# Kernel tuning notes

Hardware: AMD Instinct MI355X
Metric: run time of the kernel (lower is better)

The kernel has to match this reference:

```python
import jax, jax.numpy as jnp
import numpy as np

B, C, P, H, W, S = 4, 256, 128, 56, 56, 5
EPS = 1e-5


def setup_inputs() -> dict:
    key = jax.random.key(0)
    ks = jax.random.split(key, 6)
    return {
        "x": jax.random.normal(ks[0], (B, C, H, W), jnp.float32),
        "Wt": jax.random.normal(ks[1], (P, C), jnp.float32) * 0.05,
        "Wp": jax.random.normal(ks[2], (P, C), jnp.float32) * 0.05,
        "Wg": jax.random.normal(ks[3], (S, P, C), jnp.float32) * 0.05,
        "W1": jax.random.normal(ks[4], (S, C, P), jnp.float32) * 0.05,
        "W2": jax.random.normal(ks[5], (S, C, P), jnp.float32) * 0.05,
        "gamma": jnp.ones((S, C), jnp.float32),
        "beta": jnp.zeros((S, C), jnp.float32),
    }


def _batchnorm(o, g, b):
    # training-mode BN over (batch, spatial); o: [b, C, n]
    mean = o.mean(axis=(0, 2), keepdims=True)
    var = ((o - mean) ** 2).mean(axis=(0, 2), keepdims=True)
    return (o - mean) * jax.lax.rsqrt(var + EPS) * g[None, :, None] + b[None, :, None]


def reference(x, Wt, Wp, Wg, W1, W2, gamma, beta):
    b, c, h, w = x.shape
    n = h * w
    xf = x.reshape(b, c, n)
    # 1x1 conv projections == channel matmuls
    t = jax.nn.relu(jnp.einsum('pc,bcn->bpn', Wt, xf))  # is_norm branch uses relu
    p = jax.nn.relu(jnp.einsum('pc,bcn->bpn', Wp, xf))
    att = jnp.einsum('bpi,bpj->bij', t, p)              # [b, n, n] affinity
    att = 0.5 * (att + jnp.swapaxes(att, 1, 2))         # is_sys symmetrization
    d = att.sum(axis=2)                                  # degree [b, n]
    d_safe = jnp.where(d != 0, d, 1.0)
    d_inv = jnp.where(d != 0, jax.lax.rsqrt(d_safe), 0.0)
    att = att * d_inv[:, None, :] * d_inv[:, :, None]    # D^-1/2 A D^-1/2
    out = xf
    for s in range(S):  # fixed small stage count
        g = jnp.einsum('pc,bcn->bpn', Wg[s], out)        # [b, P, n]
        ag = jnp.einsum('bij,bpj->bpi', att, g)          # att @ g over spatial
        o = jnp.einsum('cp,bpn->bcn', W1[s], ag) + jnp.einsum('cp,bpn->bcn', W2[s], g)
        out = _batchnorm(o, gamma[s], beta[s]) + out     # BN + residual
    return out.reshape(b, c, h, w)
```

## Files before the change

kernel.cpp:

```cpp
#include <hip/hip_runtime.h>

namespace {

constexpr int Bc = 4;
constexpr int Cc = 256;
constexpr int Pc = 128;
constexpr int NcT = 3136;
constexpr int Np = 3200;
constexpr int Sc = 5;
constexpr int KSn = 5;
constexpr int KCH = 640;
constexpr float EPSc = 1e-5f;

typedef __attribute__((ext_vector_type(8))) short bf16x8;
typedef __attribute__((ext_vector_type(4))) float f32x4;
typedef __attribute__((ext_vector_type(8))) unsigned short u16x8;
typedef __attribute__((ext_vector_type(4))) unsigned short u16x4;

__device__ inline float bf2f(unsigned short u) {
    return __uint_as_float(((unsigned)u) << 16);
}
__device__ inline unsigned short f2bf(float f) {
    unsigned u = __float_as_uint(f);
    return (unsigned short)((u + 0x7FFFu + ((u >> 16) & 1u)) >> 16);
}

template <int MT, int EPI, int CMOUT, bool SPLITK, int BNSTAT, bool F32OUT,
          bool FUSEBN>
__global__ __launch_bounds__(256) void mgemm(
    const unsigned short* __restrict__ A, int lda, long aB,
    const unsigned short* __restrict__ Bw, int ldb, long bB,
    unsigned short* __restrict__ outSM, int ldsm, long smB, long smSlice,
    unsigned short* __restrict__ outCM, long cmB,
    float* __restrict__ ps, float* __restrict__ ps2,
    int K, int kchunk, const float* __restrict__ dinv,
    const unsigned short* __restrict__ oin, const float* __restrict__ bnsc,
    const float* __restrict__ bnsh, float* __restrict__ resid)
{
    constexpr int TBA = MT * 64 * 2;
    constexpr int TBB = 128 * 64 * 2;
    constexpr int BUF = TBA + TBB;
    constexpr int OTB = MT * 132 * 4;
    constexpr int LDSZ = (2 * BUF > OTB + 2048) ? 2 * BUF : (OTB + 2048);
    __shared__ __align__(16) char lds[LDSZ];

    int b, kstart, kend;
    long smOff;
    if (SPLITK) {
        b = blockIdx.z & 3;
        int ks = blockIdx.z >> 2;
        kstart = ks * kchunk;
        kend = kstart + kchunk;
        smOff = (long)ks * smSlice;
    } else {
        b = blockIdx.z; kstart = 0; kend = K; smOff = 0;
    }
    const int n0 = blockIdx.x * 128;
    const int m0 = blockIdx.y * MT;
    const int tid = threadIdx.x;
    const int w = tid >> 6, l = tid & 63;

    const unsigned short* Ab = A + (size_t)b * aB + (size_t)m0 * lda;
    const unsigned short* Bb = Bw + (size_t)b * bB + (size_t)n0 * ldb;

    const int srow8 = tid >> 3;
    const int sgran = tid & 7;
    const int sswz = (sgran ^ (srow8 & 7)) * 8;
    constexpr int AR = MT / 32;

    constexpr int WC = (MT == 128) ? 2 : 4;
    constexpr int NB = 128 / WC / 16;
    const int wr = w / WC, wc = w % WC;

    f32x4 acc[4][NB] = {};
    float fup[AR][8];

    auto stageA = [&](int buf, int k0) {
        char* base = lds + buf * BUF;
#pragma unroll
        for (int j = 0; j < AR; ++j)
            __builtin_amdgcn_global_load_lds(
                (const __attribute__((address_space(1))) void*)
                    (Ab + (size_t)(j * 32 + srow8) * lda + k0 + sswz),
                (__attribute__((address_space(3))) void*)(base + j * 4096 + tid * 16),
                16, 0, 0);
    };
    auto stageB = [&](int buf, int k0) {
        char* base = lds + buf * BUF + TBA;
#pragma unroll
        for (int j = 0; j < 4; ++j)
            __builtin_amdgcn_global_load_lds(
                (const __attribute__((address_space(1))) void*)
                    (Bb + (size_t)(j * 32 + srow8) * ldb + k0 + sswz),
                (__attribute__((address_space(3))) void*)(base + j * 4096 + tid * 16),
                16, 0, 0);
    };
    auto fbLoad = [&](int k0) {
        const float* scp = bnsc + k0 + sgran * 8;
        const float* shp = bnsh + k0 + sgran * 8;
        float4 s0 = *(const float4*)scp, s1 = *(const float4*)(scp + 4);
        float4 h0 = *(const float4*)shp, h1 = *(const float4*)(shp + 4);
#pragma unroll
        for (int j = 0; j < AR; ++j) {
            int row = j * 32 + srow8;
            int n = m0 + row;
            size_t off = ((size_t)b * Np + n) * 256 + k0 + sgran * 8;
            if (n < NcT) {
                u16x8 ov = *(const u16x8*)(oin + off);
                float4 r0 = *(const float4*)(resid + off);
                float4 r1 = *(const float4*)(resid + off + 4);
                fup[j][0] = r0.x + fmaf(bf2f(ov[0]), s0.x, h0.x);
                fup[j][1] = r0.y + fmaf(bf2f(ov[1]), s0.y, h0.y);
                fup[j][2] = r0.z + fmaf(bf2f(ov[2]), s0.z, h0.z);
                fup[j][3] = r0.w + fmaf(bf2f(ov[3]), s0.w, h0.w);
                fup[j][4] = r1.x + fmaf(bf2f(ov[4]), s1.x, h1.x);
                fup[j][5] = r1.y + fmaf(bf2f(ov[5]), s1.y, h1.y);
                fup[j][6] = r1.z + fmaf(bf2f(ov[6]), s1.z, h1.z);
                fup[j][7] = r1.w + fmaf(bf2f(ov[7]), s1.w, h1.w);
            } else {
#pragma unroll
                for (int i = 0; i < 8; ++i) fup[j][i] = 0.f;
            }
            float4 w0, w1;
            w0.x = fup[j][0]; w0.y = fup[j][1]; w0.z = fup[j][2]; w0.w = fup[j][3];
            w1.x = fup[j][4]; w1.y = fup[j][5]; w1.z = fup[j][6]; w1.w = fup[j][7];
            *(float4*)(resid + off) = w0;
            *(float4*)(resid + off + 4) = w1;
        }
    };
    auto fbWrite = [&](int buf) {
        char* base = lds + buf * BUF;
#pragma unroll
        for (int j = 0; j < AR; ++j) {
            int row = j * 32 + srow8;
            u16x8 hv;
#pragma unroll
            for (int i = 0; i < 8; ++i) hv[i] = f2bf(fup[j][i]);
            *(u16x8*)(base + row * 128 + ((sgran ^ (row & 7)) << 4)) = hv;
        }
    };

    auto compute = [&](int buf) {
        const char* base = lds + buf * BUF;
        const int lo = l & 15, gq = l >> 4;
#pragma unroll
        for (int kh = 0; kh < 2; ++kh) {
            const int lg = kh * 4 + gq;
            bf16x8 bf[NB];
#pragma unroll
            for (int c = 0; c < NB; ++c) {
                int brow = wc * (16 * NB) + c * 16 + lo;
                bf[c] = *(const bf16x8*)(base + TBA + brow * 128 +
                                         ((lg ^ (brow & 7)) << 4));
            }
#pragma unroll
            for (int r = 0; r < 4; ++r) {
                int arow = wr * 64 + r * 16 + lo;
                bf16x8 af = *(const bf16x8*)(base + arow * 128 +
                                             ((lg ^ (arow & 7)) << 4));
#pragma unroll
                for (int c = 0; c < NB; ++c)
                    acc[r][c] = __builtin_amdgcn_mfma_f32_16x16x32_bf16(
                        af, bf[c], acc[r][c], 0, 0, 0);
            }
        }
    };

    const int nst = (kend - kstart) >> 6;
    if constexpr (FUSEBN) {
        fbLoad(kstart);
        fbWrite(0);
        stageB(0, kstart);
        __syncthreads();
        for (int s = 0; s < nst; ++s) {
            if (s + 1 < nst) {
                fbLoad(kstart + ((s + 1) << 6));
                stageB((s + 1) & 1, kstart + ((s + 1) << 6));
            }
            compute(s & 1);
            if (s + 1 < nst) fbWrite((s + 1) & 1);
            __syncthreads();
        }
    } else {
        stageA(0, kstart);
        stageB(0, kstart);
        __syncthreads();
        for (int s = 0; s < nst; ++s) {
            if (s + 1 < nst) {
                stageA((s + 1) & 1, kstart + ((s + 1) << 6));
                stageB((s + 1) & 1, kstart + ((s + 1) << 6));
            }
            compute(s & 1);
            __syncthreads();
        }
    }

    float* ot = (float*)lds;
    {
        const int lo = l & 15, gq = l >> 4;
#pragma unroll
        for (int r = 0; r < 4; ++r)
#pragma unroll
            for (int c = 0; c < NB; ++c)
#pragma unroll
                for (int j = 0; j < 4; ++j) {
                    float v = acc[r][c][j];
                    if (EPI == 1) v = fmaxf(v, 0.f);
                    ot[(wr * 64 + r * 16 + gq * 4 + j) * 132 +
                       wc * (16 * NB) + c * 16 + lo] = v;
                }
    }
    __syncthreads();

    {
        constexpr int TPR = 256 / MT;
        const int r = tid / TPR;
        const int c0 = (tid % TPR) * (MT / 2);
        if (F32OUT) {
            float* dst = (float*)outSM + (size_t)b * smB + smOff +
                         (size_t)(m0 + r) * ldsm + n0 + c0;
#pragma unroll
            for (int k = 0; k < MT / 8; ++k) {
                float4 v;
                v.x = ot[r * 132 + c0 + 4 * k + 0];
                v.y = ot[r * 132 + c0 + 4 * k + 1];
                v.z = ot[r * 132 + c0 + 4 * k + 2];
                v.w = ot[r * 132 + c0 + 4 * k + 3];
                *(float4*)(dst + 4 * k) = v;
            }
        } else {
            float sc = 1.f;
            if (EPI == 2) sc = 0.5f * dinv[(size_t)b * Np + m0 + r];
            unsigned short* dst = outSM + (size_t)b * smB + smOff +
                                  (size_t)(m0 + r) * ldsm + n0 + c0;
#pragma unroll
            for (int k = 0; k < MT / 16; ++k) {
                u16x8 o;
#pragma unroll
                for (int j = 0; j < 8; ++j) {
                    float v = ot[r * 132 + c0 + 8 * k + j];
                    if (EPI == 2) v *= sc;
                    o[j] = f2bf(v);
                }
                *(u16x8*)(dst + 8 * k) = o;
            }
        }
    }

    if (CMOUT) {
        const int c = tid >> 1, r0 = (tid & 1) * (MT / 2);
        const float* dv = dinv + (size_t)b * Np + m0 + r0;
        unsigned short* dst = outCM + (size_t)b * cmB + (size_t)(n0 + c) * Np +
                              m0 + r0;
#pragma unroll
        for (int k = 0; k < MT / 16; ++k) {
            u16x8 o;
#pragma unroll
            for (int j = 0; j < 8; ++j) {
                float v = ot[(r0 + 8 * k + j) * 132 + c];
                if (CMOUT == 2) v *= dv[8 * k + j];
                o[j] = f2bf(v);
            }
            *(u16x8*)(dst + 8 * k) = o;
        }
    }

    if (BNSTAT) {
        float* p1 = (float*)(lds + OTB);
        float* p2 = p1 + 256;
        const int col = tid & 127, half = tid >> 7;
        float s = 0.f, s2 = 0.f;
#pragma unroll
        for (int i = 0; i < MT / 2; ++i) {
            float v = ot[(half * (MT / 2) + i) * 132 + col];
            s += v;
            if (BNSTAT == 2) s2 = fmaf(v, v, s2);
        }
        p1[half * 128 + col] = s;
        if (BNSTAT == 2) p2[half * 128 + col] = s2;
        __syncthreads();
        if (tid < 128) {
            float a = p1[tid] + p1[128 + tid];
            size_t slot = ((size_t)b * gridDim.y + blockIdx.y) * 256 + n0 + tid;
            ps[slot] = a;
            if (BNSTAT == 2) ps2[slot] = p2[tid] + p2[128 + tid];
        }
    }
}

__global__ __launch_bounds__(256) void cvtw_k(
    const float* __restrict__ Wt, const float* __restrict__ Wp,
    const float* __restrict__ Wg, const float* __restrict__ W1,
    const float* __restrict__ W2,
    unsigned short* __restrict__ Wcomb, unsigned short* __restrict__ Wgh,
    unsigned short* __restrict__ Wcat)
{
    size_t e = ((size_t)blockIdx.x * 256 + threadIdx.x) * 4;
    const float* src; unsigned short* dst;
    if (e < 32768)      { src = Wt + e;           dst = Wcomb + e; }
    else if (e < 65536) { src = Wp + (e - 32768); dst = Wcomb + e; }
    else if (e < 65536 + 163840) {
        size_t o = e - 65536; src = Wg + o; dst = Wgh + o;
    } else if (e < 65536 + 2 * 163840) {
        size_t o = e - 65536 - 163840; src = W1 + o;
        dst = Wcat + ((o >> 7) << 8) + (o & 127);
    } else {
        size_t o = e - 65536 - 327680; src = W2 + o;
        dst = Wcat + ((o >> 7) << 8) + 128 + (o & 127);
    }
    float4 v = *(const float4*)src;
    u16x4 t;
    t[0] = f2bf(v.x); t[1] = f2bf(v.y); t[2] = f2bf(v.z); t[3] = f2bf(v.w);
    *(u16x4*)dst = t;
}

__global__ __launch_bounds__(256) void xpin_k(
    const float* __restrict__ x, float* __restrict__ out_sm,
    unsigned short* __restrict__ outh)
{
    __shared__ float tb[64][65];
    int b = blockIdx.z, c0 = blockIdx.y * 64, n0 = blockIdx.x * 64;
    int t = threadIdx.x;
    const bool pad = (n0 >= NcT);
    if (!pad) {
        int ci = t >> 2, nb = (t & 3) * 16;
        const float* src = x + ((size_t)b * Cc + c0 + ci) * NcT + n0 + nb;
#pragma unroll
        for (int k = 0; k < 4; ++k) {
            float4 v = *(const float4*)(src + 4 * k);
            tb[ci][nb + 4 * k + 0] = v.x; tb[ci][nb + 4 * k + 1] = v.y;
            tb[ci][nb + 4 * k + 2] = v.z; tb[ci][nb + 4 * k + 3] = v.w;
        }
    }
    __syncthreads();
    int r = t >> 2, cb = (t & 3) * 16;
    size_t off = ((size_t)b * Np + n0 + r) * 256 + c0 + cb;
    float vv[16];
#pragma unroll
    for (int j = 0; j < 16; ++j) vv[j] = pad ? 0.f : tb[cb + j][r];
    float* dst = out_sm + off;
#pragma unroll
    for (int k = 0; k < 4; ++k) {
        float4 v; v.x = vv[4*k]; v.y = vv[4*k+1]; v.z = vv[4*k+2]; v.w = vv[4*k+3];
        *(float4*)(dst + 4 * k) = v;
    }
    u16x8 h1, h2;
#pragma unroll
    for (int j = 0; j < 8; ++j) { h1[j] = f2bf(vv[j]); h2[j] = f2bf(vv[8 + j]); }
    unsigned short* dh = outh + off;
    *(u16x8*)dh = h1;
    *(u16x8*)(dh + 8) = h2;
}

__global__ __launch_bounds__(256) void xpoutbn_k(
    const float* __restrict__ out_sm, const unsigned short* __restrict__ oin,
    const float* __restrict__ scale, const float* __restrict__ shift,
    float* __restrict__ outp)
{
    __shared__ float tb[64][65];
    __shared__ float lsc[64], lsh[64];
    int b = blockIdx.z, c0 = blockIdx.y * 64, n0 = blockIdx.x * 64;
    int t = threadIdx.x;
    if (t < 64) { lsc[t] = scale[c0 + t]; lsh[t] = shift[c0 + t]; }
    __syncthreads();
    {
        int r = t >> 2, cb = (t & 3) * 16;
        size_t off = ((size_t)b * Np + n0 + r) * 256 + c0 + cb;
#pragma unroll
        for (int k = 0; k < 2; ++k) {
            float4 a0 = *(const float4*)(out_sm + off + 8 * k);
            float4 a1 = *(const float4*)(out_sm + off + 8 * k + 4);
            u16x8 ov = *(const u16x8*)(oin + off + 8 * k);
            tb[r][cb + 8*k + 0] = a0.x + fmaf(bf2f(ov[0]), lsc[cb + 8*k + 0], lsh[cb + 8*k + 0]);
            tb[r][cb + 8*k + 1] = a0.y + fmaf(bf2f(ov[1]), lsc[cb + 8*k + 1], lsh[cb + 8*k + 1]);
            tb[r][cb + 8*k + 2] = a0.z + fmaf(bf2f(ov[2]), lsc[cb + 8*k + 2], lsh[cb + 8*k + 2]);
            tb[r][cb + 8*k + 3] = a0.w + fmaf(bf2f(ov[3]), lsc[cb + 8*k + 3], lsh[cb + 8*k + 3]);
            tb[r][cb + 8*k + 4] = a1.x + fmaf(bf2f(ov[4]), lsc[cb + 8*k + 4], lsh[cb + 8*k + 4]);
            tb[r][cb + 8*k + 5] = a1.y + fmaf(bf2f(ov[5]), lsc[cb + 8*k + 5], lsh[cb + 8*k + 5]);
            tb[r][cb + 8*k + 6] = a1.z + fmaf(bf2f(ov[6]), lsc[cb + 8*k + 6], lsh[cb + 8*k + 6]);
            tb[r][cb + 8*k + 7] = a1.w + fmaf(bf2f(ov[7]), lsc[cb + 8*k + 7], lsh[cb + 8*k + 7]);
        }
    }
    __syncthreads();
    {
        int c = t >> 2, rb = (t & 3) * 16;
        float vv[16];
#pragma unroll
        for (int j = 0; j < 16; ++j) vv[j] = tb[rb + j][c];
        float* dst = outp + ((size_t)b * Cc + c0 + c) * NcT + n0 + rb;
#pragma unroll
        for (int k = 0; k < 4; ++k) {
            float4 v; v.x = vv[4*k]; v.y = vv[4*k+1]; v.z = vv[4*k+2]; v.w = vv[4*k+3];
            *(float4*)(dst + 4 * k) = v;
        }
    }
}

__global__ __launch_bounds__(256) void dinv_k(
    const unsigned short* __restrict__ U, const float* __restrict__ rp,
    float* __restrict__ dinv)
{
    __shared__ float rsl[256];
    int b = blockIdx.y, tid = threadIdx.x;
    float s = 0.f;
    for (int j = 0; j < 25; ++j) s += rp[((size_t)b * 25 + j) * 256 + tid];
    rsl[tid ^ 128] = s;
    __syncthreads();
    int i = blockIdx.x * 256 + tid;
    if (i < Np) {
        const unsigned short* row = U + ((size_t)b * Np + i) * 256;
        float acc = 0.f;
        for (int q0 = 0; q0 < 256; q0 += 8) {
            u16x8 v = *(const u16x8*)(row + q0);
#pragma unroll
            for (int j = 0; j < 8; ++j) acc = fmaf(bf2f(v[j]), rsl[q0 + j], acc);
        }
        float d = 0.5f * acc;
        dinv[(size_t)b * Np + i] = d > 0.f ? rsqrtf(d) : 0.f;
    }
}

__global__ __launch_bounds__(256) void redmst_k(
    const float* __restrict__ Cpart, unsigned short* __restrict__ MstT)
{
    int e8 = blockIdx.x * 256 + threadIdx.x;
    int bp = e8 >> 5, qc = e8 & 31;
    size_t dstOff = ((size_t)bp * 32 + qc) * 8;
    size_t srcOff = ((size_t)bp * 32 + (qc ^ 16)) * 8;
    float4 s0 = {0.f, 0.f, 0.f, 0.f}, s1 = {0.f, 0.f, 0.f, 0.f};
    for (int ks = 0; ks < KSn; ++ks) {
        const float* base = Cpart + (size_t)ks * (Bc * Pc * Cc) + srcOff;
        float4 v0 = *(const float4*)base;
        float4 v1 = *(const float4*)(base + 4);
        s0.x += v0.x; s0.y += v0.y; s0.z += v0.z; s0.w += v0.w;
        s1.x += v1.x; s1.y += v1.y; s1.z += v1.z; s1.w += v1.w;
    }
    u16x8 o;
    o[0] = f2bf(s0.x); o[1] = f2bf(s0.y); o[2] = f2bf(s0.z); o[3] = f2bf(s0.w);
    o[4] = f2bf(s1.x); o[5] = f2bf(s1.y); o[6] = f2bf(s1.z); o[7] = f2bf(s1.w);
    *(u16x8*)(MstT + dstOff) = o;
}

__global__ __launch_bounds__(256) void bnfin_k(
    const float* __restrict__ ps, const float* __restrict__ ps2,
    const float* __restrict__ gamma, const float* __restrict__ beta,
    float* __restrict__ scale, float* __restrict__ shift)
{
    __shared__ float l1[256], l2[256];
    int t = threadIdx.x;
    int c = blockIdx.x * 16 + (t & 15);
    int gl = t >> 4;
    float a = 0.f, a2 = 0.f;
    for (int g = gl; g < 100; g += 16) {
        a += ps[(size_t)g * 256 + c];
        a2 += ps2[(size_t)g * 256 + c];
    }
    l1[t] = a; l2[t] = a2;
    __syncthreads();
    if (gl == 0) {
#pragma unroll
        for (int j = 1; j < 16; ++j) {
            a += l1[j * 16 + (t & 15)];
            a2 += l2[j * 16 + (t & 15)];
        }
        const float inv = 1.f / (float)(Bc * NcT);
        float mean = a * inv;
        float var = a2 * inv - mean * mean;
        float sc = gamma[c] * rsqrtf(var + EPSc);
        scale[c] = sc;
        shift[c] = beta[c] - mean * sc;
    }
}

}

extern "C" void kernel_launch(void* const* d_in, const int* in_sizes, int n_in,
                              void* d_out, int out_size, void* d_ws, size_t ws_size,
                              hipStream_t stream) {
    const float* x     = (const float*)d_in[0];
    const float* Wt    = (const float*)d_in[1];
    const float* Wp    = (const float*)d_in[2];
    const float* Wg    = (const float*)d_in[3];
    const float* W1    = (const float*)d_in[4];
    const float* W2    = (const float*)d_in[5];
    const float* gamma = (const float*)d_in[6];
    const float* beta  = (const float*)d_in[7];

    char* p = (char*)d_ws;
    auto alloc = [&](size_t bytes) { char* r = p; p += (bytes + 255) & ~(size_t)255; return r; };
    float*          out_sm = (float*)         alloc((size_t)Bc * Np * 256 * 4);
    unsigned short* outh   = (unsigned short*)alloc((size_t)Bc * Np * 256 * 2);
    unsigned short* U_sm   = (unsigned short*)alloc((size_t)Bc * Np * 256 * 2);
    unsigned short* U_cm   = (unsigned short*)alloc((size_t)Bc * 256 * Np * 2);
    unsigned short* agg    = (unsigned short*)alloc((size_t)Bc * Np * 256 * 2);
    unsigned short* g_cmd  = (unsigned short*)alloc((size_t)Bc * Pc * Np * 2);
    unsigned short* o_sm   = (unsigned short*)alloc((size_t)Bc * Np * 256 * 2);
    float*          Cpart  = (float*)         alloc((size_t)KSn * Bc * Pc * Cc * 4);
    unsigned short* MstT   = (unsigned short*)alloc((size_t)Bc * Pc * Cc * 2);
    unsigned short* Wcomb  = (unsigned short*)alloc((size_t)Cc * Cc * 2);
    unsigned short* Wgh    = (unsigned short*)alloc((size_t)Sc * Pc * Cc * 2);
    unsigned short* Wcat   = (unsigned short*)alloc((size_t)Sc * Cc * 256 * 2);
    float*          rp     = (float*)         alloc((size_t)100 * 256 * 4);
    float*          dinv   = (float*)         alloc((size_t)Bc * Np * 4);
    float*          ps     = (float*)         alloc((size_t)100 * 256 * 4);
    float*          ps2    = (float*)         alloc((size_t)100 * 256 * 4);
    float*          scale  = (float*)         alloc(256 * 4);
    float*          shiftb = (float*)         alloc(256 * 4);

    const long NpC = (long)Np * 256;
    dim3 blk(256);

    cvtw_k<<<544, blk, 0, stream>>>(Wt, Wp, Wg, W1, W2, Wcomb, Wgh, Wcat);
    xpin_k<<<dim3(50, 4, Bc), blk, 0, stream>>>(x, out_sm, outh);

    mgemm<128, 1, 1, false, 1, false, false><<<dim3(2, 25, Bc), blk, 0, stream>>>(
        outh, 256, NpC, Wcomb, 256, 0,
        U_sm, 256, NpC, 0, U_cm, (long)256 * Np, rp, nullptr,
        256, 0, nullptr, nullptr, nullptr, nullptr, nullptr);

    dinv_k<<<dim3(13, Bc), blk, 0, stream>>>(U_sm, rp, dinv);

    for (int s = 0; s < Sc; ++s) {
        if (s == 0)
            mgemm<64, 0, 2, false, 0, false, false><<<dim3(1, 50, Bc), blk, 0, stream>>>(
                outh, 256, NpC, Wgh, 256, 0,
                agg + 128, 256, NpC, 0, g_cmd, (long)Pc * Np, nullptr, nullptr,
                256, 0, dinv, nullptr, nullptr, nullptr, nullptr);
        else
            mgemm<64, 0, 2, false, 0, false, true><<<dim3(1, 50, Bc), blk, 0, stream>>>(
                outh, 256, NpC, Wgh + (size_t)s * Pc * Cc, 256, 0,
                agg + 128, 256, NpC, 0, g_cmd, (long)Pc * Np, nullptr, nullptr,
                256, 0, dinv, o_sm, scale, shiftb, out_sm);
        mgemm<64, 0, 0, true, 0, true, false><<<dim3(2, 2, KSn * Bc), blk, 0, stream>>>(
            g_cmd, Np, (long)Pc * Np, U_cm, Np, (long)256 * Np,
            (unsigned short*)Cpart, 256, (long)Pc * Cc, (long)Bc * Pc * Cc,
            nullptr, 0, nullptr, nullptr, Np, KCH, nullptr,
            nullptr, nullptr, nullptr, nullptr);
        redmst_k<<<64, blk, 0, stream>>>(Cpart, MstT);
        mgemm<64, 2, 0, false, 0, false, false><<<dim3(1, 50, Bc), blk, 0, stream>>>(
            U_sm, 256, NpC, MstT, 256, (long)Pc * Cc,
            agg, 256, NpC, 0, nullptr, 0, nullptr, nullptr,
            256, 0, dinv, nullptr, nullptr, nullptr, nullptr);
        mgemm<128, 0, 0, false, 2, false, false><<<dim3(2, 25, Bc), blk, 0, stream>>>(
            agg, 256, NpC, Wcat + (size_t)s * Cc * 256, 256, 0,
            o_sm, 256, NpC, 0, nullptr, 0, ps, ps2,
            256, 0, nullptr, nullptr, nullptr, nullptr, nullptr);
        bnfin_k<<<16, blk, 0, stream>>>(ps, ps2, gamma + s * Cc, beta + s * Cc,
                                        scale, shiftb);
    }

    xpoutbn_k<<<dim3(49, 4, Bc), blk, 0, stream>>>(out_sm, o_sm, scale, shiftb,
                                                   (float*)d_out);
}
```

Before: 264.9 us.

## Reassociate per-stage graph aggregation through a small weight-folded matrix with dual-K GEMM

The stage no longer builds the full aggregated activation. It computes Cpart = U^T g split over K, then folds W1 into it to form a small per-batch 256x256 matrix WMb. It then produces o from a single dual-K GEMM, Ud·WMb plus g·W2, which also collects BN statistics. This removes the redmst reduction kernel, the agg intermediate and the separate concat-weight GEMM, and the weight conversion and input transpose are merged into one prep kernel. The cost is an extra GEMM launch, a new dinv-scaled Ud buffer computed once, and bf16 partial sums in Cpart, which may reduce precision.

```diff
diff --git a/kernel.cpp b/kernel.cpp
--- a/kernel.cpp
+++ b/kernel.cpp
@@ -25,17 +25,23 @@
     return (unsigned short)((u + 0x7FFFu + ((u >> 16) & 1u)) >> 16);
 }
 
-template <int MT, int EPI, int CMOUT, bool SPLITK, int BNSTAT, bool F32OUT,
-          bool FUSEBN>
-__global__ __launch_bounds__(256) void mgemm(
-    const unsigned short* __restrict__ A, int lda, long aB,
-    const unsigned short* __restrict__ Bw, int ldb, long bB,
-    unsigned short* __restrict__ outSM, int ldsm, long smB, long smSlice,
-    unsigned short* __restrict__ outCM, long cmB,
-    float* __restrict__ ps, float* __restrict__ ps2,
-    int K, int kchunk, const float* __restrict__ dinv,
-    const unsigned short* __restrict__ oin, const float* __restrict__ bnsc,
-    const float* __restrict__ bnsh, float* __restrict__ resid)
+struct GP {
+    const unsigned short* A; int lda; long aB; long aSl;
+    const unsigned short* Bw; int ldb; long bB; long bSl;
+    const unsigned short* A2; int lda2; long aB2;
+    const unsigned short* B2; int ldb2; long bB2;
+    int K; int K2; int nsl; int kchunk;
+    unsigned short* outSM; int ldsm; long smB; long smSlice;
+    unsigned short* outCM; long cmB;
+    float* ps; float* ps2;
+    const float* dinv;
+    const unsigned short* oin; const float* bnsc; const float* bnsh;
+    float* resid;
+};
+
+template <int MT, int EPI, int CMOUT, bool SPLITK, int BNSTAT, bool FUSEBN,
+          bool XORM, bool DUALK>
+__global__ __launch_bounds__(256) void mgemm(GP p)
 {
     constexpr int TBA = MT * 64 * 2;
     constexpr int TBB = 128 * 64 * 2;
@@ -44,24 +50,23 @@
     constexpr int LDSZ = (2 * BUF > OTB + 2048) ? 2 * BUF : (OTB + 2048);
     __shared__ __align__(16) char lds[LDSZ];
 
-    int b, kstart, kend;
+    int b, kstart;
     long smOff;
     if (SPLITK) {
         b = blockIdx.z & 3;
         int ks = blockIdx.z >> 2;
-        kstart = ks * kchunk;
-        kend = kstart + kchunk;
-        smOff = (long)ks * smSlice;
+        kstart = ks * p.kchunk;
+        smOff = (long)ks * p.smSlice;
     } else {
-        b = blockIdx.z; kstart = 0; kend = K; smOff = 0;
+        b = blockIdx.z; kstart = 0; smOff = 0;
     }
     const int n0 = blockIdx.x * 128;
     const int m0 = blockIdx.y * MT;
     const int tid = threadIdx.x;
     const int w = tid >> 6, l = tid & 63;
 
-    const unsigned short* Ab = A + (size_t)b * aB + (size_t)m0 * lda;
-    const unsigned short* Bb = Bw + (size_t)b * bB + (size_t)n0 * ldb;
+    const unsigned short* Ab = p.A + (size_t)b * p.aB + (size_t)m0 * p.lda;
+    const unsigned short* Bb = p.Bw + (size_t)b * p.bB + (size_t)n0 * p.ldb;
 
     const int srow8 = tid >> 3;
     const int sgran = tid & 7;
@@ -75,29 +80,41 @@
     f32x4 acc[4][NB] = {};
     float fup[AR][8];
 
-    auto stageA = [&](int buf, int k0) {
+    auto stage1 = [&](int buf, int sl, int k0) {
         char* base = lds + buf * BUF;
+        const unsigned short* As = Ab + (size_t)sl * p.aSl + k0 + sswz;
 #pragma unroll
         for (int j = 0; j < AR; ++j)
             __builtin_amdgcn_global_load_lds(
                 (const __attribute__((address_space(1))) void*)
-                    (Ab + (size_t)(j * 32 + srow8) * lda + k0 + sswz),
+                    (As + (size_t)(j * 32 + srow8) * p.lda),
+                (__attribute__((address_space(3))) void*)(base + j * 4096 + tid * 16),
+                16, 0, 0);
+        const unsigned short* Bs = Bb + (size_t)sl * p.bSl + k0 + sswz;
+#pragma unroll
+        for (int j = 0; j < 4; ++j)
+            __builtin_amdgcn_global_load_lds(
+                (const __attribute__((address_space(1))) void*)
+                    (Bs + (size_t)(j * 32 + srow8) * p.ldb),
+                (__attribute__((address_space(3))) void*)(base + TBA + j * 4096 + tid * 16),
+                16, 0, 0);
+    };
+
+    auto stageB1 = [&](int buf, int k0) {
+        char* base = lds + buf * BUF + TBA;
+        const unsigned short* Bs = Bb + k0 + sswz;
+#pragma unroll
+        for (int j = 0; j < 4; ++j)
+            __builtin_amdgcn_global_load_lds(
+                (const __attribute__((address_space(1))) void*)
+                    (Bs + (size_t)(j * 32 + srow8) * p.ldb),
                 (__attribute__((address_space(3))) void*)(base + j * 4096 + tid * 16),
                 16, 0, 0);
     };
-    auto stageB = [&](int buf, int k0) {
-        char* base = lds + buf * BUF + TBA;
-#pragma unroll
-        for (int j = 0; j < 4; ++j)
-            __builtin_amdgcn_global_load_lds(
-                (const __attribute__((address_space(1))) void*)
-                    (Bb + (size_t)(j * 32 + srow8) * ldb + k0 + sswz),
-                (__attribute__((address_space(3))) void*)(base + j * 4096 + tid * 16),
-                16, 0, 0);
-    };
+
     auto fbLoad = [&](int k0) {
-        const float* scp = bnsc + k0 + sgran * 8;
-        const float* shp = bnsh + k0 + sgran * 8;
+        const float* scp = p.bnsc + k0 + sgran * 8;
+        const float* shp = p.bnsh + k0 + sgran * 8;
         float4 s0 = *(const float4*)scp, s1 = *(const float4*)(scp + 4);
         float4 h0 = *(const float4*)shp, h1 = *(const float4*)(shp + 4);
 #pragma unroll
@@ -106,9 +123,9 @@
             int n = m0 + row;
             size_t off = ((size_t)b * Np + n) * 256 + k0 + sgran * 8;
             if (n < NcT) {
-                u16x8 ov = *(const u16x8*)(oin + off);
-                float4 r0 = *(const float4*)(resid + off);
-                float4 r1 = *(const float4*)(resid + off + 4);
+                u16x8 ov = *(const u16x8*)(p.oin + off);
+                float4 r0 = *(const float4*)(p.resid + off);
+                float4 r1 = *(const float4*)(p.resid + off + 4);
                 fup[j][0] = r0.x + fmaf(bf2f(ov[0]), s0.x, h0.x);
                 fup[j][1] = r0.y + fmaf(bf2f(ov[1]), s0.y, h0.y);
                 fup[j][2] = r0.z + fmaf(bf2f(ov[2]), s0.z, h0.z);
@@ -117,15 +134,15 @@
                 fup[j][5] = r1.y + fmaf(bf2f(ov[5]), s1.y, h1.y);
                 fup[j][6] = r1.z + fmaf(bf2f(ov[6]), s1.z, h1.z);
                 fup[j][7] = r1.w + fmaf(bf2f(ov[7]), s1.w, h1.w);
+                float4 w0, w1;
+                w0.x = fup[j][0]; w0.y = fup[j][1]; w0.z = fup[j][2]; w0.w = fup[j][3];
+                w1.x = fup[j][4]; w1.y = fup[j][5]; w1.z = fup[j][6]; w1.w = fup[j][7];
+                *(float4*)(p.resid + off) = w0;
+                *(float4*)(p.resid + off + 4) = w1;
             } else {
 #pragma unroll
                 for (int i = 0; i < 8; ++i) fup[j][i] = 0.f;
             }
-            float4 w0, w1;
-            w0.x = fup[j][0]; w0.y = fup[j][1]; w0.z = fup[j][2]; w0.w = fup[j][3];
-            w1.x = fup[j][4]; w1.y = fup[j][5]; w1.z = fup[j][6]; w1.w = fup[j][7];
-            *(float4*)(resid + off) = w0;
-            *(float4*)(resid + off + 4) = w1;
         }
     };
     auto fbWrite = [&](int buf) {
@@ -166,31 +183,65 @@
         }
     };
 
-    const int nst = (kend - kstart) >> 6;
     if constexpr (FUSEBN) {
+        const int nst = p.K >> 6;
         fbLoad(kstart);
         fbWrite(0);
-        stageB(0, kstart);
+        stageB1(0, kstart);
         __syncthreads();
         for (int s = 0; s < nst; ++s) {
             if (s + 1 < nst) {
                 fbLoad(kstart + ((s + 1) << 6));
-                stageB((s + 1) & 1, kstart + ((s + 1) << 6));
+                stageB1((s + 1) & 1, kstart + ((s + 1) << 6));
             }
             compute(s & 1);
             if (s + 1 < nst) fbWrite((s + 1) & 1);
             __syncthreads();
         }
     } else {
-        stageA(0, kstart);
-        stageB(0, kstart);
+        const int nsteps1 = (SPLITK ? p.kchunk : p.K) >> 6;
+        const int spl2 = DUALK ? (p.K2 >> 6) : 0;
+        const int tot = p.nsl * nsteps1 + spl2;
+
+        const unsigned short* Ab2 = DUALK ?
+            (p.A2 + (size_t)b * p.aB2 + (size_t)m0 * p.lda2) : nullptr;
+        const unsigned short* Bb2 = DUALK ?
+            (p.B2 + (size_t)b * p.bB2 + (size_t)n0 * p.ldb2) : nullptr;
+        auto stage2 = [&](int buf, int k0) {
+            if constexpr (DUALK) {
+                char* base = lds + buf * BUF;
+                const unsigned short* As = Ab2 + k0 + sswz;
+#pragma unroll
+                for (int j = 0; j < AR; ++j)
+                    __builtin_amdgcn_global_load_lds(
+                        (const __attribute__((address_space(1))) void*)
+                            (As + (size_t)(j * 32 + srow8) * p.lda2),
+                        (__attribute__((address_space(3))) void*)(base + j * 4096 + tid * 16),
+                        16, 0, 0);
+                const unsigned short* Bs = Bb2 + k0 + sswz;
+#pragma unroll
+                for (int j = 0; j < 4; ++j)
+                    __builtin_amdgcn_global_load_lds(
+                        (const __attribute__((address_space(1))) void*)
+                            (Bs + (size_t)(j * 32 + srow8) * p.ldb2),
+                        (__attribute__((address_space(3))) void*)(base + TBA + j * 4096 + tid * 16),
+                        16, 0, 0);
+            }
+        };
+
+        stage1(0, 0, kstart);
         __syncthreads();
-        for (int s = 0; s < nst; ++s) {
-            if (s + 1 < nst) {
-                stageA((s + 1) & 1, kstart + ((s + 1) << 6));
-                stageB((s + 1) & 1, kstart + ((s + 1) << 6));
+        int sl = 0, st = 1;
+        if (st == nsteps1) { st = 0; sl = 1; }
+        for (int gs = 0; gs < tot; ++gs) {
+            if (gs + 1 < tot) {
+                if (sl < p.nsl) stage1((gs + 1) & 1, sl, kstart + (st << 6));
+                else            stage2((gs + 1) & 1, st << 6);
+                ++st;
+                int lim = (sl < p.nsl) ? nsteps1 : spl2;
+                if (st == lim) { st = 0; ++sl; }
             }
-            compute(s & 1);
+            compute(gs & 1);
             __syncthreads();
         }
     }
@@ -216,42 +267,23 @@
         constexpr int TPR = 256 / MT;
         const int r = tid / TPR;
         const int c0 = (tid % TPR) * (MT / 2);
-        if (F32OUT) {
-            float* dst = (float*)outSM + (size_t)b * smB + smOff +
-                         (size_t)(m0 + r) * ldsm + n0 + c0;
-#pragma unroll
-            for (int k = 0; k < MT / 8; ++k) {
-                float4 v;
-                v.x = ot[r * 132 + c0 + 4 * k + 0];
-                v.y = ot[r * 132 + c0 + 4 * k + 1];
-                v.z = ot[r * 132 + c0 + 4 * k + 2];
-                v.w = ot[r * 132 + c0 + 4 * k + 3];
-                *(float4*)(dst + 4 * k) = v;
-            }
-        } else {
-            float sc = 1.f;
-            if (EPI == 2) sc = 0.5f * dinv[(size_t)b * Np + m0 + r];
-            unsigned short* dst = outSM + (size_t)b * smB + smOff +
-                                  (size_t)(m0 + r) * ldsm + n0 + c0;
-#pragma unroll
-            for (int k = 0; k < MT / 16; ++k) {
-                u16x8 o;
-#pragma unroll
-                for (int j = 0; j < 8; ++j) {
-                    float v = ot[r * 132 + c0 + 8 * k + j];
-                    if (EPI == 2) v *= sc;
-                    o[j] = f2bf(v);
-                }
-                *(u16x8*)(dst + 8 * k) = o;
-            }
+        const int m0s = XORM ? (m0 ^ 128) : m0;
+        unsigned short* dst = p.outSM + (size_t)b * p.smB + smOff +
+                              (size_t)(m0s + r) * p.ldsm + n0 + c0;
+#pragma unroll
+        for (int k = 0; k < MT / 16; ++k) {
+            u16x8 o;
+#pragma unroll
+            for (int j = 0; j < 8; ++j) o[j] = f2bf(ot[r * 132 + c0 + 8 * k + j]);
+            *(u16x8*)(dst + 8 * k) = o;
         }
     }
 
     if (CMOUT) {
         const int c = tid >> 1, r0 = (tid & 1) * (MT / 2);
-        const float* dv = dinv + (size_t)b * Np + m0 + r0;
-        unsigned short* dst = outCM + (size_t)b * cmB + (size_t)(n0 + c) * Np +
-                              m0 + r0;
+        const float* dv = p.dinv + (size_t)b * Np + m0 + r0;
+        unsigned short* dst = p.outCM + (size_t)b * p.cmB +
+                              (size_t)(n0 + c) * Np + m0 + r0;
 #pragma unroll
         for (int k = 0; k < MT / 16; ++k) {
             u16x8 o;
@@ -280,47 +312,42 @@
         if (BNSTAT == 2) p2[half * 128 + col] = s2;
         __syncthreads();
         if (tid < 128) {
-            float a = p1[tid] + p1[128 + tid];
+            float aa = p1[tid] + p1[128 + tid];
             size_t slot = ((size_t)b * gridDim.y + blockIdx.y) * 256 + n0 + tid;
-            ps[slot] = a;
-            if (BNSTAT == 2) ps2[slot] = p2[tid] + p2[128 + tid];
-        }
-    }
-}
-
-__global__ __launch_bounds__(256) void cvtw_k(
-    const float* __restrict__ Wt, const float* __restrict__ Wp,
-    const float* __restrict__ Wg, const float* __restrict__ W1,
-    const float* __restrict__ W2,
+            p.ps[slot] = aa;
+            if (BNSTAT == 2) p.ps2[slot] = p2[tid] + p2[128 + tid];
+        }
+    }
+}
+
+__global__ __launch_bounds__(256) void prep_k(
+    const float* __restrict__ x, const float* __restrict__ Wt,
+    const float* __restrict__ Wp, const float* __restrict__ Wg,
+    const float* __restrict__ W1, const float* __restrict__ W2,
     unsigned short* __restrict__ Wcomb, unsigned short* __restrict__ Wgh,
-    unsigned short* __restrict__ Wcat)
-{
-    size_t e = ((size_t)blockIdx.x * 256 + threadIdx.x) * 4;
-    const float* src; unsigned short* dst;
-    if (e < 32768)      { src = Wt + e;           dst = Wcomb + e; }
-    else if (e < 65536) { src = Wp + (e - 32768); dst = Wcomb + e; }
-    else if (e < 65536 + 163840) {
-        size_t o = e - 65536; src = Wg + o; dst = Wgh + o;
-    } else if (e < 65536 + 2 * 163840) {
-        size_t o = e - 65536 - 163840; src = W1 + o;
-        dst = Wcat + ((o >> 7) << 8) + (o & 127);
-    } else {
-        size_t o = e - 65536 - 327680; src = W2 + o;
-        dst = Wcat + ((o >> 7) << 8) + 128 + (o & 127);
-    }
-    float4 v = *(const float4*)src;
-    u16x4 t;
-    t[0] = f2bf(v.x); t[1] = f2bf(v.y); t[2] = f2bf(v.z); t[3] = f2bf(v.w);
-    *(u16x4*)dst = t;
-}
-
-__global__ __launch_bounds__(256) void xpin_k(
-    const float* __restrict__ x, float* __restrict__ out_sm,
-    unsigned short* __restrict__ outh)
+    unsigned short* __restrict__ W1h, unsigned short* __restrict__ W2h,
+    float* __restrict__ out_sm, unsigned short* __restrict__ outh)
 {
     __shared__ float tb[64][65];
-    int b = blockIdx.z, c0 = blockIdx.y * 64, n0 = blockIdx.x * 64;
+    int item = blockIdx.x;
     int t = threadIdx.x;
+    if (item < 544) {
+        size_t e = ((size_t)item * 256 + t) * 4;
+        const float* src; unsigned short* dst;
+        if (e < 32768)       { src = Wt + e;           dst = Wcomb + e; }
+        else if (e < 65536)  { src = Wp + (e - 32768); dst = Wcomb + e; }
+        else if (e < 229376) { size_t o = e - 65536;  src = Wg + o; dst = Wgh + o; }
+        else if (e < 393216) { size_t o = e - 229376; src = W1 + o; dst = W1h + o; }
+        else                 { size_t o = e - 393216; src = W2 + o; dst = W2h + o; }
+        float4 v = *(const float4*)src;
+        u16x4 t4;
+        t4[0] = f2bf(v.x); t4[1] = f2bf(v.y); t4[2] = f2bf(v.z); t4[3] = f2bf(v.w);
+        *(u16x4*)dst = t4;
+        return;
+    }
+    int it = item - 544;
+    int nx = it % 50, cy = (it / 50) % 4, b = it / 200;
+    int c0 = cy * 64, n0 = nx * 64;
     const bool pad = (n0 >= NcT);
     if (!pad) {
         int ci = t >> 2, nb = (t & 3) * 16;
@@ -350,50 +377,6 @@
     unsigned short* dh = outh + off;
     *(u16x8*)dh = h1;
     *(u16x8*)(dh + 8) = h2;
-}
-
-__global__ __launch_bounds__(256) void xpoutbn_k(
-    const float* __restrict__ out_sm, const unsigned short* __restrict__ oin,
-    const float* __restrict__ scale, const float* __restrict__ shift,
-    float* __restrict__ outp)
-{
-    __shared__ float tb[64][65];
-    __shared__ float lsc[64], lsh[64];
-    int b = blockIdx.z, c0 = blockIdx.y * 64, n0 = blockIdx.x * 64;
-    int t = threadIdx.x;
-    if (t < 64) { lsc[t] = scale[c0 + t]; lsh[t] = shift[c0 + t]; }
-    __syncthreads();
-    {
-        int r = t >> 2, cb = (t & 3) * 16;
-        size_t off = ((size_t)b * Np + n0 + r) * 256 + c0 + cb;
-#pragma unroll
-        for (int k = 0; k < 2; ++k) {
-            float4 a0 = *(const float4*)(out_sm + off + 8 * k);
-            float4 a1 = *(const float4*)(out_sm + off + 8 * k + 4);
-            u16x8 ov = *(const u16x8*)(oin + off + 8 * k);
-            tb[r][cb + 8*k + 0] = a0.x + fmaf(bf2f(ov[0]), lsc[cb + 8*k + 0], lsh[cb + 8*k + 0]);
-            tb[r][cb + 8*k + 1] = a0.y + fmaf(bf2f(ov[1]), lsc[cb + 8*k + 1], lsh[cb + 8*k + 1]);
-            tb[r][cb + 8*k + 2] = a0.z + fmaf(bf2f(ov[2]), lsc[cb + 8*k + 2], lsh[cb + 8*k + 2]);
-            tb[r][cb + 8*k + 3] = a0.w + fmaf(bf2f(ov[3]), lsc[cb + 8*k + 3], lsh[cb + 8*k + 3]);
-            tb[r][cb + 8*k + 4] = a1.x + fmaf(bf2f(ov[4]), lsc[cb + 8*k + 4], lsh[cb + 8*k + 4]);
-            tb[r][cb + 8*k + 5] = a1.y + fmaf(bf2f(ov[5]), lsc[cb + 8*k + 5], lsh[cb + 8*k + 5]);
-            tb[r][cb + 8*k + 6] = a1.z + fmaf(bf2f(ov[6]), lsc[cb + 8*k + 6], lsh[cb + 8*k + 6]);
-            tb[r][cb + 8*k + 7] = a1.w + fmaf(bf2f(ov[7]), lsc[cb + 8*k + 7], lsh[cb + 8*k + 7]);
-        }
-    }
-    __syncthreads();
-    {
-        int c = t >> 2, rb = (t & 3) * 16;
-        float vv[16];
-#pragma unroll
-        for (int j = 0; j < 16; ++j) vv[j] = tb[rb + j][c];
-        float* dst = outp + ((size_t)b * Cc + c0 + c) * NcT + n0 + rb;
-#pragma unroll
-        for (int k = 0; k < 4; ++k) {
-            float4 v; v.x = vv[4*k]; v.y = vv[4*k+1]; v.z = vv[4*k+2]; v.w = vv[4*k+3];
-            *(float4*)(dst + 4 * k) = v;
-        }
-    }
 }
 
 __global__ __launch_bounds__(256) void dinv_k(
@@ -420,25 +403,17 @@
     }
 }
 
-__global__ __launch_bounds__(256) void redmst_k(
-    const float* __restrict__ Cpart, unsigned short* __restrict__ MstT)
+__global__ __launch_bounds__(256) void ud_k(
+    const unsigned short* __restrict__ U, const float* __restrict__ dinv,
+    unsigned short* __restrict__ Ud)
 {
-    int e8 = blockIdx.x * 256 + threadIdx.x;
-    int bp = e8 >> 5, qc = e8 & 31;
-    size_t dstOff = ((size_t)bp * 32 + qc) * 8;
-    size_t srcOff = ((size_t)bp * 32 + (qc ^ 16)) * 8;
-    float4 s0 = {0.f, 0.f, 0.f, 0.f}, s1 = {0.f, 0.f, 0.f, 0.f};
-    for (int ks = 0; ks < KSn; ++ks) {
-        const float* base = Cpart + (size_t)ks * (Bc * Pc * Cc) + srcOff;
-        float4 v0 = *(const float4*)base;
-        float4 v1 = *(const float4*)(base + 4);
-        s0.x += v0.x; s0.y += v0.y; s0.z += v0.z; s0.w += v0.w;
-        s1.x += v1.x; s1.y += v1.y; s1.z += v1.z; s1.w += v1.w;
-    }
+    size_t e = ((size_t)blockIdx.x * 256 + threadIdx.x) * 8;
+    float sc = 0.5f * dinv[e >> 8];
+    u16x8 v = *(const u16x8*)(U + e);
     u16x8 o;
-    o[0] = f2bf(s0.x); o[1] = f2bf(s0.y); o[2] = f2bf(s0.z); o[3] = f2bf(s0.w);
-    o[4] = f2bf(s1.x); o[5] = f2bf(s1.y); o[6] = f2bf(s1.z); o[7] = f2bf(s1.w);
-    *(u16x8*)(MstT + dstOff) = o;
+#pragma unroll
+    for (int j = 0; j < 8; ++j) o[j] = f2bf(bf2f(v[j]) * sc);
+    *(u16x8*)(Ud + e) = o;
 }
 
 __global__ __launch_bounds__(256) void bnfin_k(
@@ -472,6 +447,50 @@
     }
 }
 
+__global__ __launch_bounds__(256) void xpoutbn_k(
+    const float* __restrict__ out_sm, const unsigned short* __restrict__ oin,
+    const float* __restrict__ scale, const float* __restrict__ shift,
+    float* __restrict__ outp)
+{
+    __shared__ float tb[64][65];
+    __shared__ float lsc[64], lsh[64];
+    int b = blockIdx.z, c0 = blockIdx.y * 64, n0 = blockIdx.x * 64;
+    int t = threadIdx.x;
+    if (t < 64) { lsc[t] = scale[c0 + t]; lsh[t] = shift[c0 + t]; }
+    __syncthreads();
+    {
+        int r = t >> 2, cb = (t & 3) * 16;
+        size_t off = ((size_t)b * Np + n0 + r) * 256 + c0 + cb;
+#pragma unroll
+        for (int k = 0; k < 2; ++k) {
+            float4 a0 = *(const float4*)(out_sm + off + 8 * k);
+            float4 a1 = *(const float4*)(out_sm + off + 8 * k + 4);
+            u16x8 ov = *(const u16x8*)(oin + off + 8 * k);
+            tb[r][cb + 8*k + 0] = a0.x + fmaf(bf2f(ov[0]), lsc[cb + 8*k + 0], lsh[cb + 8*k + 0]);
+            tb[r][cb + 8*k + 1] = a0.y + fmaf(bf2f(ov[1]), lsc[cb + 8*k + 1], lsh[cb + 8*k + 1]);
+            tb[r][cb + 8*k + 2] = a0.z + fmaf(bf2f(ov[2]), lsc[cb + 8*k + 2], lsh[cb + 8*k + 2]);
+            tb[r][cb + 8*k + 3] = a0.w + fmaf(bf2f(ov[3]), lsc[cb + 8*k + 3], lsh[cb + 8*k + 3]);
+            tb[r][cb + 8*k + 4] = a1.x + fmaf(bf2f(ov[4]), lsc[cb + 8*k + 4], lsh[cb + 8*k + 4]);
+            tb[r][cb + 8*k + 5] = a1.y + fmaf(bf2f(ov[5]), lsc[cb + 8*k + 5], lsh[cb + 8*k + 5]);
+            tb[r][cb + 8*k + 6] = a1.z + fmaf(bf2f(ov[6]), lsc[cb + 8*k + 6], lsh[cb + 8*k + 6]);
+            tb[r][cb + 8*k + 7] = a1.w + fmaf(bf2f(ov[7]), lsc[cb + 8*k + 7], lsh[cb + 8*k + 7]);
+        }
+    }
+    __syncthreads();
+    {
+        int c = t >> 2, rb = (t & 3) * 16;
+        float vv[16];
+#pragma unroll
+        for (int j = 0; j < 16; ++j) vv[j] = tb[rb + j][c];
+        float* dst = outp + ((size_t)b * Cc + c0 + c) * NcT + n0 + rb;
+#pragma unroll
+        for (int k = 0; k < 4; ++k) {
+            float4 v; v.x = vv[4*k]; v.y = vv[4*k+1]; v.z = vv[4*k+2]; v.w = vv[4*k+3];
+            *(float4*)(dst + 4 * k) = v;
+        }
+    }
+}
+
 }
 
 extern "C" void kernel_launch(void* const* d_in, const int* in_sizes, int n_in,
@@ -492,14 +511,16 @@
     unsigned short* outh   = (unsigned short*)alloc((size_t)Bc * Np * 256 * 2);
     unsigned short* U_sm   = (unsigned short*)alloc((size_t)Bc * Np * 256 * 2);
     unsigned short* U_cm   = (unsigned short*)alloc((size_t)Bc * 256 * Np * 2);
-    unsigned short* agg    = (unsigned short*)alloc((size_t)Bc * Np * 256 * 2);
+    unsigned short* Ud     = (unsigned short*)alloc((size_t)Bc * Np * 256 * 2);
+    unsigned short* g_sm   = (unsigned short*)alloc((size_t)Bc * Np * Pc * 2);
     unsigned short* g_cmd  = (unsigned short*)alloc((size_t)Bc * Pc * Np * 2);
     unsigned short* o_sm   = (unsigned short*)alloc((size_t)Bc * Np * 256 * 2);
-    float*          Cpart  = (float*)         alloc((size_t)KSn * Bc * Pc * Cc * 4);
-    unsigned short* MstT   = (unsigned short*)alloc((size_t)Bc * Pc * Cc * 2);
+    unsigned short* Cpart  = (unsigned short*)alloc((size_t)KSn * Bc * 256 * Pc * 2);
+    unsigned short* WMb    = (unsigned short*)alloc((size_t)Bc * Cc * 256 * 2);
     unsigned short* Wcomb  = (unsigned short*)alloc((size_t)Cc * Cc * 2);
     unsigned short* Wgh    = (unsigned short*)alloc((size_t)Sc * Pc * Cc * 2);
-    unsigned short* Wcat   = (unsigned short*)alloc((size_t)Sc * Cc * 256 * 2);
+    unsigned short* W1h    = (unsigned short*)alloc((size_t)Sc * Cc * Pc * 2);
+    unsigned short* W2h    = (unsigned short*)alloc((size_t)Sc * Cc * Pc * 2);
     float*          rp     = (float*)         alloc((size_t)100 * 256 * 4);
     float*          dinv   = (float*)         alloc((size_t)Bc * Np * 4);
     float*          ps     = (float*)         alloc((size_t)100 * 256 * 4);
@@ -510,41 +531,74 @@
     const long NpC = (long)Np * 256;
     dim3 blk(256);
 
-    cvtw_k<<<544, blk, 0, stream>>>(Wt, Wp, Wg, W1, W2, Wcomb, Wgh, Wcat);
-    xpin_k<<<dim3(50, 4, Bc), blk, 0, stream>>>(x, out_sm, outh);
-
-    mgemm<128, 1, 1, false, 1, false, false><<<dim3(2, 25, Bc), blk, 0, stream>>>(
-        outh, 256, NpC, Wcomb, 256, 0,
-        U_sm, 256, NpC, 0, U_cm, (long)256 * Np, rp, nullptr,
-        256, 0, nullptr, nullptr, nullptr, nullptr, nullptr);
+    prep_k<<<1344, blk, 0, stream>>>(x, Wt, Wp, Wg, W1, W2,
+                                     Wcomb, Wgh, W1h, W2h, out_sm, outh);
+
+    {
+        GP g{};
+        g.A = outh; g.lda = 256; g.aB = NpC; g.aSl = 0;
+        g.Bw = Wcomb; g.ldb = 256; g.bB = 0; g.bSl = 0;
+        g.K = 256; g.nsl = 1;
+        g.outSM = U_sm; g.ldsm = 256; g.smB = NpC; g.smSlice = 0;
+        g.outCM = U_cm; g.cmB = (long)256 * Np;
+        g.ps = rp;
+        mgemm<128, 1, 1, false, 1, false, false, false>
+            <<<dim3(2, 25, Bc), blk, 0, stream>>>(g);
+    }
 
     dinv_k<<<dim3(13, Bc), blk, 0, stream>>>(U_sm, rp, dinv);
+    ud_k<<<1600, blk, 0, stream>>>(U_sm, dinv, Ud);
 
     for (int s = 0; s < Sc; ++s) {
-        if (s == 0)
-            mgemm<64, 0, 2, false, 0, false, false><<<dim3(1, 50, Bc), blk, 0, stream>>>(
-                outh, 256, NpC, Wgh, 256, 0,
-                agg + 128, 256, NpC, 0, g_cmd, (long)Pc * Np, nullptr, nullptr,
-                256, 0, dinv, nullptr, nullptr, nullptr, nullptr);
-        else
-            mgemm<64, 0, 2, false, 0, false, true><<<dim3(1, 50, Bc), blk, 0, stream>>>(
-                outh, 256, NpC, Wgh + (size_t)s * Pc * Cc, 256, 0,
-                agg + 128, 256, NpC, 0, g_cmd, (long)Pc * Np, nullptr, nullptr,
-                256, 0, dinv, o_sm, scale, shiftb, out_sm);
-        mgemm<64, 0, 0, true, 0, true, false><<<dim3(2, 2, KSn * Bc), blk, 0, stream>>>(
-            g_cmd, Np, (long)Pc * Np, U_cm, Np, (long)256 * Np,
-            (unsigned short*)Cpart, 256, (long)Pc * Cc, (long)Bc * Pc * Cc,
-            nullptr, 0, nullptr, nullptr, Np, KCH, nullptr,
-            nullptr, nullptr, nullptr, nullptr);
-        redmst_k<<<64, blk, 0, stream>>>(Cpart, MstT);
-        mgemm<64, 2, 0, false, 0, false, false><<<dim3(1, 50, Bc), blk, 0, stream>>>(
-            U_sm, 256, NpC, MstT, 256, (long)Pc * Cc,
-            agg, 256, NpC, 0, nullptr, 0, nullptr, nullptr,
-            256, 0, dinv, nullptr, nullptr, nullptr, nullptr);
-        mgemm<128, 0, 0, false, 2, false, false><<<dim3(2, 25, Bc), blk, 0, stream>>>(
-            agg, 256, NpC, Wcat + (size_t)s * Cc * 256, 256, 0,
-            o_sm, 256, NpC, 0, nullptr, 0, ps, ps2,
-            256, 0, nullptr, nullptr, nullptr, nullptr, nullptr);
+        {
+            GP g{};
+            g.A = outh; g.lda = 256; g.aB = NpC; g.aSl = 0;
+            g.Bw = Wgh + (size_t)s * Pc * Cc; g.ldb = 256; g.bB = 0; g.bSl = 0;
+            g.K = 256; g.nsl = 1;
+            g.outSM = g_sm; g.ldsm = 128; g.smB = (long)Np * 128; g.smSlice = 0;
+            g.outCM = g_cmd; g.cmB = (long)Pc * Np;
+            g.dinv = dinv;
+            g.oin = o_sm; g.bnsc = scale; g.bnsh = shiftb; g.resid = out_sm;
+            if (s == 0)
+                mgemm<64, 0, 2, false, 0, false, false, false>
+                    <<<dim3(1, 50, Bc), blk, 0, stream>>>(g);
+            else
+                mgemm<64, 0, 2, false, 0, true, false, false>
+                    <<<dim3(1, 50, Bc), blk, 0, stream>>>(g);
+        }
+        {
+            GP g{};
+            g.A = U_cm; g.lda = Np; g.aB = (long)256 * Np; g.aSl = 0;
+            g.Bw = g_cmd; g.ldb = Np; g.bB = (long)Pc * Np; g.bSl = 0;
+            g.K = Np; g.kchunk = KCH; g.nsl = 1;
+            g.outSM = Cpart; g.ldsm = 128; g.smB = (long)256 * Pc;
+            g.smSlice = (long)Bc * 256 * Pc;
+            mgemm<64, 0, 0, true, 0, false, true, false>
+                <<<dim3(1, 4, KSn * Bc), blk, 0, stream>>>(g);
+        }
+        {
+            GP g{};
+            g.A = W1h + (size_t)s * Cc * Pc; g.lda = 128; g.aB = 0; g.aSl = 0;
+            g.Bw = Cpart; g.ldb = 128; g.bB = (long)256 * Pc;
+            g.bSl = (long)Bc * 256 * Pc;
+            g.K = 128; g.nsl = KSn;
+            g.outSM = WMb; g.ldsm = 256; g.smB = (long)Cc * 256; g.smSlice = 0;
+            mgemm<64, 0, 0, false, 0, false, false, false>
+                <<<dim3(2, 4, Bc), blk, 0, stream>>>(g);
+        }
+        {
+            GP g{};
+            g.A = Ud; g.lda = 256; g.aB = NpC; g.aSl = 0;
+            g.Bw = WMb; g.ldb = 256; g.bB = (long)Cc * 256; g.bSl = 0;
+            g.K = 256; g.nsl = 1;
+            g.A2 = g_sm; g.lda2 = 128; g.aB2 = (long)Np * 128;
+            g.B2 = W2h + (size_t)s * Cc * Pc; g.ldb2 = 128; g.bB2 = 0;
+            g.K2 = 128;
+            g.outSM = o_sm; g.ldsm = 256; g.smB = NpC; g.smSlice = 0;
+            g.ps = ps; g.ps2 = ps2;
+            mgemm<128, 0, 0, false, 2, false, false, true>
+                <<<dim3(2, 25, Bc), blk, 0, stream>>>(g);
+        }
         bnfin_k<<<16, blk, 0, stream>>>(ps, ps2, gamma + s * Cc, beta + s * Cc,
                                         scale, shiftb);
     }
```

After: 271.0 us. 1.02x slower.
